# Performance work log

Measured on AMD Instinct MI355X. Metric: run time of the kernel, lower is better.

## Reference

```python
import jax, jax.numpy as jnp
import numpy as np
from jax import lax

K = 8  # window / output_stride (hardcoded in original forward)
BN_EPS = 1e-5


def setup_inputs() -> dict:
    key = jax.random.key(0)
    ks = jax.random.split(key, 4)
    B, C, H, W = 4, 56, 320, 320
    return {
        "x": jax.random.normal(ks[0], (B, C, H, W), jnp.float32),
        "conv1_w": jax.random.normal(ks[1], (56, 56), jnp.float32) * 0.01,
        "conv1_b": jnp.zeros((56,), jnp.float32),
        "conv2_w": jax.random.normal(ks[2], (1, 56), jnp.float32) * 0.01,
        "conv2_b": jnp.zeros((1,), jnp.float32),
        "bn1_gamma": jnp.ones((56,), jnp.float32),
        "bn1_beta": jnp.zeros((56,), jnp.float32),
        "bn2_gamma": jnp.ones((1,), jnp.float32),
        "bn2_beta": jnp.zeros((1,), jnp.float32),
    }


def _batchnorm(y, gamma, beta):
    # training-mode BatchNorm2d: stats over (N, H, W) per channel
    mean = jnp.mean(y, axis=(0, 2, 3), keepdims=True)
    var = jnp.var(y, axis=(0, 2, 3), keepdims=True)
    yhat = (y - mean) * lax.rsqrt(var + BN_EPS)
    return yhat * gamma[None, :, None, None] + beta[None, :, None, None]


def _counter(x, w1, b1, w2, b2, g1, be1, g2, be2):
    # AvgPool2d(kernel=8, stride=1) -> [B,56,H-7,W-7]
    p = lax.reduce_window(x, 0.0, lax.add, (1, 1, K, K), (1, 1, 1, 1), "VALID") / (K * K)
    y = jnp.einsum("oc,bchw->bohw", w1, p) + b1[None, :, None, None]
    y = jax.nn.relu(_batchnorm(y, g1, be1))
    y = jnp.einsum("oc,bchw->bohw", w2, y) + b2[None, :, None, None]
    y = jax.nn.relu(_batchnorm(y, g2, be2))
    return y  # [B,1,Hc,Wc]


def _dynamic_unfolding(x, local_count):
    # x: [B,C,H,W], local_count: [B,1,H-7,W-7]
    B, C, H, W = x.shape
    Hc, Wc = H - K + 1, W - K + 1
    m = jnp.mean(x, axis=1)  # [B,H,W]
    # extract all 8x8 sliding windows -> [B,Hc,Wc,64]
    patches = jnp.stack(
        [m[:, di:di + Hc, dj:dj + Wc] for di in range(K) for dj in range(K)],
        axis=-1,
    )
    sm = jax.nn.softmax(patches, axis=-1)  # per-window softmax
    wgt = sm * local_count[:, 0, :, :, None]  # [B,Hc,Wc,64]
    # overlapping fold (scatter-add) back to [B,1,H,W]
    R = jnp.zeros((B, H, W), x.dtype)
    for di in range(K):
        for dj in range(K):
            R = R.at[:, di:di + Hc, dj:dj + Wc].add(wgt[..., di * K + dj])
    return R[:, None, :, :]


def reference(x, conv1_w, conv1_b, conv2_w, conv2_b, bn1_gamma, bn1_beta, bn2_gamma, bn2_beta):
    C_out = _counter(x, conv1_w, conv1_b, conv2_w, conv2_b, bn1_gamma, bn1_beta, bn2_gamma, bn2_beta)
    R = _dynamic_unfolding(x, C_out)
    return C_out, R
```

## Files before the change

kernel.cpp:

```cpp
#include <hip/hip_runtime.h>
#include <math.h>

#define B 4
#define C 56
#define H 320
#define W 320
#define HC 313
#define WC 313
#define NIMG (H*W)
#define NSP  (HC*WC)
#define NPIX (B*NSP)
#define NM   (B*NIMG)
#define BN_EPS 1e-5f
#define NGRID 512

#define PHR 39
#define PNH (PHR*PHR)

typedef __attribute__((ext_vector_type(8))) short short8;
typedef __attribute__((ext_vector_type(16))) float float16;

__device__ __forceinline__ unsigned short f2bf(float v) {
  unsigned int u = __float_as_uint(v);
  return (unsigned short)((u + 0x7fffu + ((u >> 16) & 1u)) >> 16);
}

__global__ __launch_bounds__(256) void pool32_kernel(
    const float* __restrict__ x, float* __restrict__ Epart,
    unsigned short* __restrict__ p_t) {
  __shared__ float tin[PHR][40];
  __shared__ float hs[PHR][32];
  __shared__ unsigned short Pt[8][1024];
  const int tid = threadIdx.x;
  int bid = blockIdx.x;
  const int g = bid % 7; bid /= 7;
  const int b = bid & 3; bid >>= 2;
  const int ty = bid / 10, tx = bid - (bid / 10) * 10;
  const int i0 = ty * 32, j0 = tx * 32;
  const float* xg = x + ((size_t)b * C + g * 8) * NIMG;

  float esum[6];
  #pragma unroll
  for (int k = 0; k < 6; ++k) esum[k] = 0.f;

  float cur[6], nxt[6];
  {
    const float* xp = xg;
    #pragma unroll
    for (int k = 0; k < 6; ++k) {
      int idx = tid + k * 256;
      int r = idx / PHR, cc = idx - r * PHR;
      int gi = i0 + r, gj = j0 + cc;
      cur[k] = (idx < PNH && gi < H && gj < W) ? xp[gi * W + gj] : 0.f;
    }
  }

  #pragma unroll
  for (int c = 0; c < 8; ++c) {
    #pragma unroll
    for (int k = 0; k < 6; ++k) {
      int idx = tid + k * 256;
      if (idx < PNH) {
        int r = idx / PHR, cc = idx - r * PHR;
        tin[r][cc] = cur[k];
        if (r < 32 && cc < 32) esum[k] += cur[k];
      }
    }
    __syncthreads();
    if (c < 7) {
      const float* xp = xg + (size_t)(c + 1) * NIMG;
      #pragma unroll
      for (int k = 0; k < 6; ++k) {
        int idx = tid + k * 256;
        int r = idx / PHR, cc = idx - r * PHR;
        int gi = i0 + r, gj = j0 + cc;
        nxt[k] = (idx < PNH && gi < H && gj < W) ? xp[gi * W + gj] : 0.f;
      }
    }
    #pragma unroll
    for (int it = 0; it < 5; ++it) {
      int idx = tid + it * 256;
      if (idx < PHR * 32) {
        int r = idx >> 5, j = idx & 31;
        float s = 0.f;
        #pragma unroll
        for (int d = 0; d < 8; ++d) s += tin[r][j + d];
        hs[r][j] = s;
      }
    }
    __syncthreads();
    #pragma unroll
    for (int it = 0; it < 4; ++it) {
      int idx = tid + it * 256;
      int i = idx >> 5, j = idx & 31;
      float s = 0.f;
      #pragma unroll
      for (int d = 0; d < 8; ++d) s += hs[i + d][j];
      Pt[c][idx] = f2bf(s * (1.f / 64.f));
    }
    #pragma unroll
    for (int k = 0; k < 6; ++k) cur[k] = nxt[k];
  }
  __syncthreads();

  float* Eb = Epart + ((size_t)g * B + b) * NIMG;
  #pragma unroll
  for (int k = 0; k < 6; ++k) {
    int idx = tid + k * 256;
    if (idx < PNH) {
      int r = idx / PHR, cc = idx - r * PHR;
      if (r < 32 && cc < 32) Eb[(i0 + r) * W + (j0 + cc)] = esum[k];
    }
  }

  unsigned short* pg = p_t + (size_t)g * NPIX * 8;
  #pragma unroll
  for (int k = 0; k < 4; ++k) {
    int idx = tid + k * 256;
    int i = idx >> 5, j = idx & 31;
    int gi = i0 + i, gj = j0 + j;
    if (gi < HC && gj < WC) {
      unsigned short t8[8];
      #pragma unroll
      for (int c2 = 0; c2 < 8; ++c2) t8[c2] = Pt[c2][idx];
      *(short8*)(pg + ((size_t)b * NSP + gi * WC + gj) * 8) = *(short8*)t8;
    }
  }
}

__global__ __launch_bounds__(256) void se_pool_kernel(
    const float* __restrict__ Epart, float* __restrict__ E, float* __restrict__ S) {
  __shared__ float tin[39][40];
  __shared__ float hs[39][33];
  const int b = blockIdx.z;
  const int i0 = blockIdx.y * 32, j0 = blockIdx.x * 32;
  const int tid = threadIdx.x;
  for (int idx = tid; idx < 39 * 39; idx += 256) {
    int r = idx / 39, cc = idx - r * 39;
    int gi = i0 + r, gj = j0 + cc;
    float v = 0.f;
    if (gi < H && gj < W) {
      float s = 0.f;
      #pragma unroll
      for (int g = 0; g < 7; ++g)
        s += Epart[((size_t)g * B + b) * NIMG + gi * W + gj];
      v = expf(s * (1.f / C));
      if (r < 32 && cc < 32) E[(size_t)b * NIMG + gi * W + gj] = v;
    }
    tin[r][cc] = v;
  }
  __syncthreads();
  for (int idx = tid; idx < 39 * 32; idx += 256) {
    int r = idx >> 5, j = idx & 31;
    float s = 0.f;
    #pragma unroll
    for (int d = 0; d < 8; ++d) s += tin[r][j + d];
    hs[r][j] = s;
  }
  __syncthreads();
  for (int idx = tid; idx < 32 * 32; idx += 256) {
    int i = idx >> 5, j = idx & 31;
    int gi = i0 + i, gj = j0 + j;
    if (gi < HC && gj < WC) {
      float s = 0.f;
      #pragma unroll
      for (int d = 0; d < 8; ++d) s += hs[i + d][j];
      S[(size_t)b * NSP + gi * WC + gj] = s;
    }
  }
}

__global__ __launch_bounds__(256) void y1_stats_kernel(
    const unsigned short* __restrict__ p_t, const float* __restrict__ w1,
    float* __restrict__ ypart) {
  __shared__ unsigned short Wl[64 * 64];
  __shared__ float red[4][32][64];
  const int tid = threadIdx.x, wave = tid >> 6, lane = tid & 63;
  for (int idx = tid; idx < 4096; idx += 256) {
    int o = idx >> 6, k = idx & 63;
    float v = (o < C && k < C) ? w1[o * C + k] : 0.f;
    *(unsigned short*)((char*)Wl + (o * 128 + ((2 * k) ^ ((o & 7) << 4)))) = f2bf(v);
  }
  __syncthreads();
  short8 afr[2][4];
  #pragma unroll
  for (int q = 0; q < 2; ++q)
    #pragma unroll
    for (int ks = 0; ks < 4; ++ks) {
      int row = q * 32 + (lane & 31), kb = ks * 16 + 8 * (lane >> 5);
      afr[q][ks] = *(const short8*)((const char*)Wl + row * 128 + ((2 * kb) ^ ((row & 7) << 4)));
    }
  float s1[2][16], s2[2][16];
  #pragma unroll
  for (int q = 0; q < 2; ++q)
    #pragma unroll
    for (int r = 0; r < 16; ++r) { s1[q][r] = 0.f; s2[q][r] = 0.f; }

  const int h = lane >> 5;
  const int nchunk = (NPIX + 127) / 128;
  for (int ch = blockIdx.x; ch < nchunk; ch += NGRID) {
    int col = ch * 128 + wave * 32 + (lane & 31);
    bool cv = col < NPIX;
    size_t pofs = (size_t)(cv ? col : 0) * 8;
    short8 bfr[4];
    #pragma unroll
    for (int ks = 0; ks < 4; ++ks) {
      int g = ks * 2 + h;
      short8 bv = (short8){0, 0, 0, 0, 0, 0, 0, 0};
      if (g < 7 && cv) bv = *(const short8*)(p_t + (size_t)g * NPIX * 8 + pofs);
      bfr[ks] = bv;
    }
    float16 a0 = {}, a1 = {};
    #pragma unroll
    for (int ks = 0; ks < 4; ++ks) {
      a0 = __builtin_amdgcn_mfma_f32_32x32x16_bf16(afr[0][ks], bfr[ks], a0, 0, 0, 0);
      a1 = __builtin_amdgcn_mfma_f32_32x32x16_bf16(afr[1][ks], bfr[ks], a1, 0, 0, 0);
    }
    #pragma unroll
    for (int r = 0; r < 16; ++r) {
      s1[0][r] += a0[r]; s2[0][r] = fmaf(a0[r], a0[r], s2[0][r]);
      s1[1][r] += a1[r]; s2[1][r] = fmaf(a1[r], a1[r], s2[1][r]);
    }
  }
  for (int pass = 0; pass < 2; ++pass) {
    __syncthreads();
    #pragma unroll
    for (int q = 0; q < 2; ++q)
      #pragma unroll
      for (int r = 0; r < 16; ++r)
        red[wave][q * 16 + r][lane] = pass ? s2[q][r] : s1[q][r];
    __syncthreads();
    if (tid < C) {
      int row = tid, q = row >> 5, rr = row & 31;
      int hh = (rr >> 2) & 1, reg = (rr & 3) | ((rr >> 3) << 2);
      float s = 0.f;
      #pragma unroll
      for (int w = 0; w < 4; ++w)
        #pragma unroll
        for (int cl = 0; cl < 32; ++cl)
          s += red[w][q * 16 + reg][32 * hh + cl];
      ypart[blockIdx.x * 112 + pass * 56 + row] = s;
    }
  }
}

__global__ void ypart_bn1_kernel(const float* __restrict__ ypart,
                                 const float* __restrict__ g1, const float* __restrict__ be1,
                                 float* __restrict__ ac) {
  __shared__ float sums[112];
  int t = threadIdx.x;
  if (t < 112) {
    float s0 = 0.f, s1 = 0.f, s2 = 0.f, s3 = 0.f;
    #pragma unroll 4
    for (int b = 0; b < NGRID; b += 4) {
      s0 += ypart[(b + 0) * 112 + t];
      s1 += ypart[(b + 1) * 112 + t];
      s2 += ypart[(b + 2) * 112 + t];
      s3 += ypart[(b + 3) * 112 + t];
    }
    sums[t] = (s0 + s1) + (s2 + s3);
  }
  __syncthreads();
  if (t < C) {
    float m = sums[t] * (1.f / NPIX);
    float var = sums[56 + t] * (1.f / NPIX) - m * m;
    float a = g1[t] * rsqrtf(var + BN_EPS);
    ac[t] = a;
    ac[C + t] = fmaf(-a, m, be1[t]);
  }
}

__global__ __launch_bounds__(256) void y2_kernel(
    const unsigned short* __restrict__ p_t, const float* __restrict__ w1,
    const float* __restrict__ ac, const float* __restrict__ w2,
    float* __restrict__ y2, float* __restrict__ stats2) {
  __shared__ unsigned short Wl[64 * 64];
  __shared__ float af[64], cf[64], wf[64];
  const int tid = threadIdx.x, wave = tid >> 6, lane = tid & 63;
  for (int idx = tid; idx < 4096; idx += 256) {
    int o = idx >> 6, k = idx & 63;
    float v = (o < C && k < C) ? w1[o * C + k] : 0.f;
    *(unsigned short*)((char*)Wl + (o * 128 + ((2 * k) ^ ((o & 7) << 4)))) = f2bf(v);
  }
  if (tid < 64) {
    bool ok = tid < C;
    af[tid] = ok ? ac[tid] : 0.f;
    cf[tid] = ok ? ac[C + tid] : 0.f;
    wf[tid] = ok ? w2[tid] : 0.f;
  }
  __syncthreads();
  short8 afr[2][4];
  #pragma unroll
  for (int q = 0; q < 2; ++q)
    #pragma unroll
    for (int ks = 0; ks < 4; ++ks) {
      int row = q * 32 + (lane & 31), kb = ks * 16 + 8 * (lane >> 5);
      afr[q][ks] = *(const short8*)((const char*)Wl + row * 128 + ((2 * kb) ^ ((row & 7) << 4)));
    }
  const int h = lane >> 5;
  float ss1 = 0.f, ss2 = 0.f;
  const int nchunk = (NPIX + 127) / 128;
  for (int ch = blockIdx.x; ch < nchunk; ch += NGRID) {
    int col = ch * 128 + wave * 32 + (lane & 31);
    bool cv = col < NPIX;
    size_t pofs = (size_t)(cv ? col : 0) * 8;
    short8 bfr[4];
    #pragma unroll
    for (int ks = 0; ks < 4; ++ks) {
      int g = ks * 2 + h;
      short8 bv = (short8){0, 0, 0, 0, 0, 0, 0, 0};
      if (g < 7 && cv) bv = *(const short8*)(p_t + (size_t)g * NPIX * 8 + pofs);
      bfr[ks] = bv;
    }
    float16 a0 = {}, a1 = {};
    #pragma unroll
    for (int ks = 0; ks < 4; ++ks) {
      a0 = __builtin_amdgcn_mfma_f32_32x32x16_bf16(afr[0][ks], bfr[ks], a0, 0, 0, 0);
      a1 = __builtin_amdgcn_mfma_f32_32x32x16_bf16(afr[1][ks], bfr[ks], a1, 0, 0, 0);
    }
    float ysum = 0.f;
    #pragma unroll
    for (int r = 0; r < 16; ++r) {
      int o0 = (r & 3) + 8 * (r >> 2) + 4 * h;
      ysum = fmaf(wf[o0], fmaxf(fmaf(af[o0], a0[r], cf[o0]), 0.f), ysum);
      int o1 = o0 + 32;
      ysum = fmaf(wf[o1], fmaxf(fmaf(af[o1], a1[r], cf[o1]), 0.f), ysum);
    }
    ysum += __shfl_xor(ysum, 32);
    bool wr = cv && lane < 32;
    if (wr) {
      y2[col] = ysum;
      ss1 += ysum;
      ss2 = fmaf(ysum, ysum, ss2);
    }
  }
  #pragma unroll
  for (int off = 1; off < 64; off <<= 1) {
    ss1 += __shfl_xor(ss1, off);
    ss2 += __shfl_xor(ss2, off);
  }
  if (lane == 0) {
    atomicAdd(&stats2[(blockIdx.x & 63) * 2 + 0], ss1);
    atomicAdd(&stats2[(blockIdx.x & 63) * 2 + 1], ss2);
  }
}

__global__ void bn2_final_kernel(const float* __restrict__ stats2,
                                 const float* __restrict__ g2, const float* __restrict__ be2,
                                 float* __restrict__ a2c2) {
  int t = threadIdx.x;
  float s1 = stats2[t * 2], s2 = stats2[t * 2 + 1];
  #pragma unroll
  for (int off = 32; off > 0; off >>= 1) {
    s1 += __shfl_down(s1, off);
    s2 += __shfl_down(s2, off);
  }
  if (t == 0) {
    float mean = s1 * (1.f / NPIX);
    float var  = s2 * (1.f / NPIX) - mean * mean;
    float a = g2[0] * rsqrtf(var + BN_EPS);
    a2c2[0] = a;
    a2c2[1] = fmaf(-a, mean, be2[0]);
  }
}

__global__ __launch_bounds__(256) void r_pool_kernel(
    const float* __restrict__ y2, const float* __restrict__ S,
    const float* __restrict__ a2c2, const float* __restrict__ E,
    float* __restrict__ cout, float* __restrict__ R) {
  __shared__ float tin[39][40];
  __shared__ float hs[39][33];
  const int b = blockIdx.z;
  const int i0 = blockIdx.y * 32, j0 = blockIdx.x * 32;
  const int tid = threadIdx.x;
  const float a2 = a2c2[0], c2 = a2c2[1];
  const float* y2b = y2 + (size_t)b * NSP;
  const float* Sb  = S + (size_t)b * NSP;
  float* cb = cout + (size_t)b * NSP;
  for (int idx = tid; idx < 39 * 39; idx += 256) {
    int r = idx / 39, cc = idx - r * 39;
    int gi = i0 + r - 7, gj = j0 + cc - 7;
    float t = 0.f;
    if (gi >= 0 && gi < HC && gj >= 0 && gj < WC) {
      float v = fmaxf(fmaf(a2, y2b[gi * WC + gj], c2), 0.f);
      t = v / Sb[gi * WC + gj];
      if (r >= 7 && cc >= 7) cb[gi * WC + gj] = v;
    }
    tin[r][cc] = t;
  }
  __syncthreads();
  for (int idx = tid; idx < 39 * 32; idx += 256) {
    int r = idx >> 5, j = idx & 31;
    float s = 0.f;
    #pragma unroll
    for (int d = 0; d < 8; ++d) s += tin[r][j + d];
    hs[r][j] = s;
  }
  __syncthreads();
  for (int idx = tid; idx < 32 * 32; idx += 256) {
    int i = idx >> 5, j = idx & 31;
    size_t gofs = (size_t)b * NIMG + (i0 + i) * W + (j0 + j);
    float s = 0.f;
    #pragma unroll
    for (int d = 0; d < 8; ++d) s += hs[i + d][j];
    R[gofs] = E[gofs] * s;
  }
}

extern "C" void kernel_launch(void* const* d_in, const int* in_sizes, int n_in,
                              void* d_out, int out_size, void* d_ws, size_t ws_size,
                              hipStream_t stream) {
  const float* x   = (const float*)d_in[0];
  const float* w1  = (const float*)d_in[1];
  const float* w2  = (const float*)d_in[3];
  const float* g1  = (const float*)d_in[5];
  const float* be1 = (const float*)d_in[6];
  const float* g2  = (const float*)d_in[7];
  const float* be2 = (const float*)d_in[8];

  float* out_c = (float*)d_out;
  float* out_r = out_c + NPIX;

  unsigned short* p_t = (unsigned short*)d_ws;
  float* fbase = (float*)(p_t + (size_t)7 * NPIX * 8);
  size_t off = 0;
  float* Epart  = fbase + off; off += (size_t)7 * NM;
  float* E      = fbase + off; off += NM;
  float* Sarr   = fbase + off; off += NPIX;
  float* y2     = fbase + off; off += NPIX;
  float* ypart  = fbase + off; off += NGRID * 112;
  float* stats2 = fbase + off; off += 128;
  float* ac     = fbase + off; off += 112;
  float* a2c2   = fbase + off; off += 2;

  hipMemsetAsync(stats2, 0, 128 * sizeof(float), stream);

  pool32_kernel<<<100 * B * 7, 256, 0, stream>>>(x, Epart, p_t);

  dim3 sg(10, 10, B);
  se_pool_kernel<<<sg, 256, 0, stream>>>(Epart, E, Sarr);

  y1_stats_kernel<<<NGRID, 256, 0, stream>>>(p_t, w1, ypart);
  ypart_bn1_kernel<<<1, 128, 0, stream>>>(ypart, g1, be1, ac);
  y2_kernel<<<NGRID, 256, 0, stream>>>(p_t, w1, ac, w2, y2, stats2);
  bn2_final_kernel<<<1, 64, 0, stream>>>(stats2, g2, be2, a2c2);

  dim3 rg(10, 10, B);
  r_pool_kernel<<<rg, 256, 0, stream>>>(y2, Sarr, a2c2, E, out_c, out_r);
}
```

Measured before the change: 120.3 us.

## Vectorize pooling tile loads, widen projection grid, parallelize BN1 partial reduction

The pooling kernel now loads its 39-row halo tile as float4 vectors over 40 columns instead of scalar loads with per-element division and bounds logic. The per-pixel channel sums are now read back from shared memory rather than tracked in registers per load slot. The y1/y2 projection kernels run on 1536 blocks instead of 512, and y1 reuses its reduction buffer for the bf16 weight tile to cut shared memory use. The BN1 partial-sum reduction runs on a 112x8 thread block to absorb the larger number of partials. Reusing the buffer risks a race between waves still reading weights and others writing reductions, and the wider grid adds more partials to reduce.

```diff
diff --git a/kernel.cpp b/kernel.cpp
--- a/kernel.cpp
+++ b/kernel.cpp
@@ -12,13 +12,14 @@
 #define NPIX (B*NSP)
 #define NM   (B*NIMG)
 #define BN_EPS 1e-5f
-#define NGRID 512
+#define YGRID 1536
 
 #define PHR 39
-#define PNH (PHR*PHR)
+#define NF4 390
 
 typedef __attribute__((ext_vector_type(8))) short short8;
 typedef __attribute__((ext_vector_type(16))) float float16;
+typedef __attribute__((ext_vector_type(4))) float f32x4;
 
 __device__ __forceinline__ unsigned short f2bf(float v) {
   unsigned int u = __float_as_uint(v);
@@ -39,43 +40,33 @@
   const int i0 = ty * 32, j0 = tx * 32;
   const float* xg = x + ((size_t)b * C + g * 8) * NIMG;
 
-  float esum[6];
-  #pragma unroll
-  for (int k = 0; k < 6; ++k) esum[k] = 0.f;
-
-  float cur[6], nxt[6];
-  {
-    const float* xp = xg;
-    #pragma unroll
-    for (int k = 0; k < 6; ++k) {
-      int idx = tid + k * 256;
-      int r = idx / PHR, cc = idx - r * PHR;
-      int gi = i0 + r, gj = j0 + cc;
-      cur[k] = (idx < PNH && gi < H && gj < W) ? xp[gi * W + gj] : 0.f;
-    }
-  }
+  int r4[2], q4[2]; bool act[2], vld[2]; size_t xoff[2];
+  #pragma unroll
+  for (int k = 0; k < 2; ++k) {
+    int idx = tid + k * 256;
+    r4[k] = idx / 10; q4[k] = idx - r4[k] * 10;
+    act[k] = idx < NF4;
+    vld[k] = act[k] && (i0 + r4[k] < H) && (j0 + q4[k] * 4 < W);
+    xoff[k] = (size_t)(i0 + r4[k]) * W + j0 + q4[k] * 4;
+  }
+  f32x4 cur4[2], nxt4[2];
+  #pragma unroll
+  for (int k = 0; k < 2; ++k)
+    cur4[k] = vld[k] ? *(const f32x4*)(xg + xoff[k]) : (f32x4){0.f, 0.f, 0.f, 0.f};
+
+  float esum[4] = {0.f, 0.f, 0.f, 0.f};
 
   #pragma unroll
   for (int c = 0; c < 8; ++c) {
     #pragma unroll
-    for (int k = 0; k < 6; ++k) {
-      int idx = tid + k * 256;
-      if (idx < PNH) {
-        int r = idx / PHR, cc = idx - r * PHR;
-        tin[r][cc] = cur[k];
-        if (r < 32 && cc < 32) esum[k] += cur[k];
-      }
-    }
+    for (int k = 0; k < 2; ++k)
+      if (act[k]) *(f32x4*)&tin[r4[k]][q4[k] * 4] = cur4[k];
     __syncthreads();
     if (c < 7) {
       const float* xp = xg + (size_t)(c + 1) * NIMG;
       #pragma unroll
-      for (int k = 0; k < 6; ++k) {
-        int idx = tid + k * 256;
-        int r = idx / PHR, cc = idx - r * PHR;
-        int gi = i0 + r, gj = j0 + cc;
-        nxt[k] = (idx < PNH && gi < H && gj < W) ? xp[gi * W + gj] : 0.f;
-      }
+      for (int k = 0; k < 2; ++k)
+        nxt4[k] = vld[k] ? *(const f32x4*)(xp + xoff[k]) : (f32x4){0.f, 0.f, 0.f, 0.f};
     }
     #pragma unroll
     for (int it = 0; it < 5; ++it) {
@@ -88,6 +79,11 @@
         hs[r][j] = s;
       }
     }
+    #pragma unroll
+    for (int k = 0; k < 4; ++k) {
+      int idx = tid + k * 256;
+      esum[k] += tin[idx >> 5][idx & 31];
+    }
     __syncthreads();
     #pragma unroll
     for (int it = 0; it < 4; ++it) {
@@ -99,18 +95,15 @@
       Pt[c][idx] = f2bf(s * (1.f / 64.f));
     }
     #pragma unroll
-    for (int k = 0; k < 6; ++k) cur[k] = nxt[k];
+    for (int k = 0; k < 2; ++k) cur4[k] = nxt4[k];
   }
   __syncthreads();
 
   float* Eb = Epart + ((size_t)g * B + b) * NIMG;
   #pragma unroll
-  for (int k = 0; k < 6; ++k) {
+  for (int k = 0; k < 4; ++k) {
     int idx = tid + k * 256;
-    if (idx < PNH) {
-      int r = idx / PHR, cc = idx - r * PHR;
-      if (r < 32 && cc < 32) Eb[(i0 + r) * W + (j0 + cc)] = esum[k];
-    }
+    Eb[(i0 + (idx >> 5)) * W + j0 + (idx & 31)] = esum[k];
   }
 
   unsigned short* pg = p_t + (size_t)g * NPIX * 8;
@@ -173,8 +166,8 @@
 __global__ __launch_bounds__(256) void y1_stats_kernel(
     const unsigned short* __restrict__ p_t, const float* __restrict__ w1,
     float* __restrict__ ypart) {
-  __shared__ unsigned short Wl[64 * 64];
   __shared__ float red[4][32][64];
+  unsigned short* Wl = (unsigned short*)&red[0][0][0];
   const int tid = threadIdx.x, wave = tid >> 6, lane = tid & 63;
   for (int idx = tid; idx < 4096; idx += 256) {
     int o = idx >> 6, k = idx & 63;
@@ -198,7 +191,7 @@
 
   const int h = lane >> 5;
   const int nchunk = (NPIX + 127) / 128;
-  for (int ch = blockIdx.x; ch < nchunk; ch += NGRID) {
+  for (int ch = blockIdx.x; ch < nchunk; ch += YGRID) {
     int col = ch * 128 + wave * 32 + (lane & 31);
     bool cv = col < NPIX;
     size_t pofs = (size_t)(cv ? col : 0) * 8;
@@ -247,23 +240,23 @@
 __global__ void ypart_bn1_kernel(const float* __restrict__ ypart,
                                  const float* __restrict__ g1, const float* __restrict__ be1,
                                  float* __restrict__ ac) {
-  __shared__ float sums[112];
+  __shared__ float part[8][112];
   int t = threadIdx.x;
-  if (t < 112) {
-    float s0 = 0.f, s1 = 0.f, s2 = 0.f, s3 = 0.f;
-    #pragma unroll 4
-    for (int b = 0; b < NGRID; b += 4) {
-      s0 += ypart[(b + 0) * 112 + t];
-      s1 += ypart[(b + 1) * 112 + t];
-      s2 += ypart[(b + 2) * 112 + t];
-      s3 += ypart[(b + 3) * 112 + t];
-    }
-    sums[t] = (s0 + s1) + (s2 + s3);
-  }
-  __syncthreads();
-  if (t < C) {
-    float m = sums[t] * (1.f / NPIX);
-    float var = sums[56 + t] * (1.f / NPIX) - m * m;
+  int ty = threadIdx.y;
+  float s = 0.f;
+  for (int b = ty; b < YGRID; b += 8) s += ypart[b * 112 + t];
+  part[ty][t] = s;
+  __syncthreads();
+  if (ty == 0) {
+    float tot = 0.f;
+    #pragma unroll
+    for (int k = 0; k < 8; ++k) tot += part[k][t];
+    part[0][t] = tot;
+  }
+  __syncthreads();
+  if (ty == 0 && t < C) {
+    float m = part[0][t] * (1.f / NPIX);
+    float var = part[0][56 + t] * (1.f / NPIX) - m * m;
     float a = g1[t] * rsqrtf(var + BN_EPS);
     ac[t] = a;
     ac[C + t] = fmaf(-a, m, be1[t]);
@@ -300,7 +293,7 @@
   const int h = lane >> 5;
   float ss1 = 0.f, ss2 = 0.f;
   const int nchunk = (NPIX + 127) / 128;
-  for (int ch = blockIdx.x; ch < nchunk; ch += NGRID) {
+  for (int ch = blockIdx.x; ch < nchunk; ch += YGRID) {
     int col = ch * 128 + wave * 32 + (lane & 31);
     bool cv = col < NPIX;
     size_t pofs = (size_t)(cv ? col : 0) * 8;
@@ -428,7 +421,7 @@
   float* E      = fbase + off; off += NM;
   float* Sarr   = fbase + off; off += NPIX;
   float* y2     = fbase + off; off += NPIX;
-  float* ypart  = fbase + off; off += NGRID * 112;
+  float* ypart  = fbase + off; off += (size_t)YGRID * 112;
   float* stats2 = fbase + off; off += 128;
   float* ac     = fbase + off; off += 112;
   float* a2c2   = fbase + off; off += 2;
@@ -440,9 +433,9 @@
   dim3 sg(10, 10, B);
   se_pool_kernel<<<sg, 256, 0, stream>>>(Epart, E, Sarr);
 
-  y1_stats_kernel<<<NGRID, 256, 0, stream>>>(p_t, w1, ypart);
-  ypart_bn1_kernel<<<1, 128, 0, stream>>>(ypart, g1, be1, ac);
-  y2_kernel<<<NGRID, 256, 0, stream>>>(p_t, w1, ac, w2, y2, stats2);
+  y1_stats_kernel<<<YGRID, 256, 0, stream>>>(p_t, w1, ypart);
+  ypart_bn1_kernel<<<1, dim3(112, 8), 0, stream>>>(ypart, g1, be1, ac);
+  y2_kernel<<<YGRID, 256, 0, stream>>>(p_t, w1, ac, w2, y2, stats2);
   bn2_final_kernel<<<1, 64, 0, stream>>>(stats2, g2, be2, a2c2);
 
   dim3 rg(10, 10, B);
```

After: 186.6 us. 1.55x slower.
